# Kernel tuning notes

Hardware: AMD Instinct MI355X
Metric: run time of the kernel (lower is better)

## Reference

```python
import jax, jax.numpy as jnp
import numpy as np
from jax.scipy.special import logsumexp

V, C, S, H = 32000, 4096, 32, 512
B, T = 32, 256
NEG = jnp.float32(-1e10)  # masked_fill value used by mask_emission


def _res(x, w1, b1, w2, b2):
    # ResidualLayerOld: relu(lin1(x)); relu(lin2(h) + x)
    h = jax.nn.relu(x @ w1.T + b1)
    return jax.nn.relu(h @ w2.T + b2 + x)


def setup_inputs() -> dict:
    key = jax.random.key(0)
    ks = jax.random.split(key, 16)
    g = lambda i, shape, s=0.02: jax.random.normal(ks[i], shape, jnp.float32) * s
    return {
        "text": jax.random.randint(ks[0], (B, T), 0, V),
        "word2state": jax.random.randint(ks[1], (V, S), 0, C - 1),
        "start_emb": g(2, (C, H), 1.0),
        "start_w1": g(3, (H, H)), "start_b1": jnp.zeros((H,), jnp.float32),
        "start_w2": g(4, (H, H)), "start_b2": jnp.zeros((H,), jnp.float32),
        "start_w3": g(5, (1, H)), "start_b3": jnp.zeros((1,), jnp.float32),
        "state_emb": g(6, (C, H), 1.0),
        "trans_w1": g(7, (H, H)), "trans_b1": jnp.zeros((H,), jnp.float32),
        "trans_w2": g(8, (H, H)), "trans_b2": jnp.zeros((H,), jnp.float32),
        "next_state_proj": g(9, (C, H)),
        "preterminal_emb": g(10, (C, H), 1.0),
        "term_w1": g(11, (H, H)), "term_b1": jnp.zeros((H,), jnp.float32),
        "term_w2": g(12, (H, H)), "term_b2": jnp.zeros((H,), jnp.float32),
        "term_w3": g(13, (V, H)), "term_b3": jnp.zeros((V,), jnp.float32),
    }


def _forward(text, word2state, start_emb, start_w1, start_b1, start_w2, start_b2,
             start_w3, start_b3, state_emb, trans_w1, trans_b1, trans_w2, trans_b2,
             next_state_proj, preterminal_emb, term_w1, term_b1, term_w2, term_b2,
             term_w3, term_b3):
    ninf = -jnp.inf
    # start distribution over states [C]
    start = jax.nn.log_softmax(
        (_res(start_emb, start_w1, start_b1, start_w2, start_b2) @ start_w3.T + start_b3)[:, 0])
    # transition [C, C]: mask last column, row-normalize, mask last row (pad state)
    tl = _res(state_emb, trans_w1, trans_b1, trans_w2, trans_b2) @ next_state_proj.T
    tl = tl.at[:, -1].set(ninf)
    trans = jax.nn.log_softmax(tl, axis=-1)
    trans = jnp.where(jnp.isnan(trans), ninf, trans)
    trans = trans.at[-1, :].set(ninf)
    # emission [C, V]: sparse word2state mask, normalize over vocab
    el = _res(preterminal_emb, term_w1, term_b1, term_w2, term_b2) @ term_w3.T + term_b3
    emask = jnp.zeros((C, V), bool).at[
        word2state.reshape(-1), jnp.repeat(jnp.arange(V), S)].set(True)
    emit = jax.nn.log_softmax(jnp.where(emask, el, NEG), axis=-1)
    emit = jnp.where(jnp.isnan(emit), ninf, emit)
    emit = emit.at[-1, :].set(ninf)
    # clamp to the S states allowed for each observed word
    cs = word2state[text]                                  # [B, T, S]
    pot = trans[cs[:, :-1, :, None], cs[:, 1:, None, :]]   # [B, T-1, S, S] (cur, next)
    obs = emit[cs, text[:, :, None]]                       # [B, T, S]
    init = start[cs[:, 0]]                                 # [B, S]
    pot = pot + obs[:, 1:, None, :]                        # obs at t+1 on next axis
    pot = pot.at[:, 0].add(init[:, :, None] + obs[:, 0, :, None])
    pot = jnp.swapaxes(pot, -1, -2)                        # [B, T-1, next, prev]
    # log-domain forward scan (the fb kernel's alpha recursion)
    alpha0 = logsumexp(pot[:, 0], axis=-1)                 # [B, S]
    def step(alpha, p):
        return logsumexp(p + alpha[:, None, :], axis=-1), None
    alpha, _ = jax.lax.scan(step, alpha0, jnp.swapaxes(pot[:, 1:], 0, 1))
    return logsumexp(alpha, axis=-1).sum()                 # evidence (sum over batch)


def reference(text, word2state, start_emb, start_w1, start_b1, start_w2, start_b2,
              start_w3, start_b3, state_emb, trans_w1, trans_b1, trans_w2, trans_b2,
              next_state_proj, preterminal_emb, term_w1, term_b1, term_w2, term_b2,
              term_w3, term_b3):
    return _forward(text, word2state, start_emb, start_w1, start_b1, start_w2,
                    start_b2, start_w3, start_b3, state_emb, trans_w1, trans_b1,
                    trans_w2, trans_b2, next_state_proj, preterminal_emb, term_w1,
                    term_b1, term_w2, term_b2, term_w3, term_b3)
```

## Files before the change

kernel.cpp:

```cpp
#include <hip/hip_runtime.h>
#include <hip/hip_bf16.h>
#include <math.h>

#define NV 32000
#define NC 4096
#define NS 32
#define NH 512
#define NB 32
#define NT 256

typedef short s16x8 __attribute__((ext_vector_type(8)));
typedef float f32x4 __attribute__((ext_vector_type(4)));

__device__ __forceinline__ float wredMax(float v){
  #pragma unroll
  for (int o = 32; o; o >>= 1) v = fmaxf(v, __shfl_xor(v, o, 64));
  return v;
}
__device__ __forceinline__ float wredSum(float v){
  #pragma unroll
  for (int o = 32; o; o >>= 1) v += __shfl_xor(v, o, 64);
  return v;
}
__device__ __forceinline__ int f2ord(float f){ int i = __float_as_int(f); return i >= 0 ? i : (i ^ 0x7fffffff); }
__device__ __forceinline__ float ord2f(int i){ return __int_as_float(i >= 0 ? i : (i ^ 0x7fffffff)); }

__device__ __forceinline__ unsigned short f2bf(float x){
  unsigned int u = __float_as_uint(x);
  return (unsigned short)((u + 0x7fffu + ((u >> 16) & 1u)) >> 16);
}
__device__ __forceinline__ float bf2f(unsigned short h){
  return __uint_as_float((unsigned int)h << 16);
}

__device__ __forceinline__ void conv_body(const float* __restrict__ src,
                                          unsigned short* __restrict__ dst, int idx)
{
  const float* s = src + (size_t)idx * 8;
  float4 f0 = *(const float4*)s;
  float4 f1 = *(const float4*)(s + 4);
  float fv[8] = {f0.x, f0.y, f0.z, f0.w, f1.x, f1.y, f1.z, f1.w};
  s16x8 vh, vl;
  #pragma unroll
  for (int e = 0; e < 8; ++e) {
    unsigned short h = f2bf(fv[e]);
    vh[e] = (short)h;
    vl[e] = (short)f2bf(fv[e] - bf2f(h));
  }
  int r = idx >> 6, c8 = idx & 63;
  unsigned short* d = dst + (size_t)r * 1024 + c8 * 8;
  *(s16x8*)d = vh;
  *(s16x8*)(d + 512) = vl;
}

struct ConvArgs {
  const float* src[10];
  unsigned short* dst[10];
  int rows[10];
};

__global__ __launch_bounds__(256)
void conv_batch(ConvArgs a)
{
  int z = blockIdx.y;
  int idx = blockIdx.x * 256 + threadIdx.x;
  if (idx >= a.rows[z] * 64) return;
  conv_body(a.src[z], a.dst[z], idx);
}

__global__ __launch_bounds__(256)
void conv_single(const float* __restrict__ src, unsigned short* __restrict__ dst)
{
  int idx = blockIdx.x * 256 + threadIdx.x;
  conv_body(src, dst, idx);
}

template<int BM, bool RELU, bool BIAS, bool RES>
__global__ __launch_bounds__(256)
void gemm_bf16s(const unsigned short* __restrict__ Asp, const unsigned short* __restrict__ Bsp,
                const float* __restrict__ bias, const float* __restrict__ res,
                float* __restrict__ Co, int M, int N, int K)
{
  constexpr int BN = 128;
  constexpr int MF = BM / 32;
  constexpr int NFR = 4;
  __shared__ char smem[BM * 128 + BN * 128];
  char* smA = smem;
  char* smB = smem + BM * 128;

  const int tid  = threadIdx.x;
  const int lane = tid & 63, w = tid >> 6;
  const int wr = w >> 1, wc = w & 1;
  const int bm = blockIdx.y * BM, bn = blockIdx.x * BN;
  const int lda = 2 * K;
  const int l8 = lane >> 3, s8 = lane & 7;
  const int frow = lane & 15, kgrp = lane >> 4;

  f32x4 acc[MF][NFR] = {};

  #pragma unroll 1
  for (int seg = 0; seg < 3; ++seg) {
    const int aoff = (seg == 1) ? K : 0;
    const int boff = (seg == 2) ? K : 0;
    #pragma unroll 1
    for (int k0 = 0; k0 < K; k0 += 64) {
      #pragma unroll
      for (int c = 0; c < MF; ++c) {
        int q = w * MF + c;
        int row = q * 8 + l8;
        s16x8 v = *(const s16x8*)(Asp + (size_t)(bm + row) * lda + aoff + k0 + s8 * 8);
        unsigned int o = (unsigned int)(row * 128 + (s8 << 4));
        o ^= (unsigned int)((row & 7) << 4);
        *(s16x8*)(smA + o) = v;
      }
      #pragma unroll
      for (int c = 0; c < NFR; ++c) {
        int q = w * NFR + c;
        int row = q * 8 + l8;
        s16x8 v = *(const s16x8*)(Bsp + (size_t)(bn + row) * lda + boff + k0 + s8 * 8);
        unsigned int o = (unsigned int)(row * 128 + (s8 << 4));
        o ^= (unsigned int)((row & 7) << 4);
        *(s16x8*)(smB + o) = v;
      }
      __syncthreads();
      #pragma unroll
      for (int kk = 0; kk < 64; kk += 32) {
        s16x8 af[MF], bfr[NFR];
        #pragma unroll
        for (int im = 0; im < MF; ++im) {
          int ar = wr * (BM / 2) + im * 16 + frow;
          unsigned int o = ((unsigned int)(ar * 128 + (kk + kgrp * 8) * 2)) ^ ((unsigned int)((ar & 7) << 4));
          af[im] = *(const s16x8*)(smA + o);
        }
        #pragma unroll
        for (int jn = 0; jn < NFR; ++jn) {
          int bc = wc * 64 + jn * 16 + frow;
          unsigned int o = ((unsigned int)(bc * 128 + (kk + kgrp * 8) * 2)) ^ ((unsigned int)((bc & 7) << 4));
          bfr[jn] = *(const s16x8*)(smB + o);
        }
        #pragma unroll
        for (int im = 0; im < MF; ++im)
          #pragma unroll
          for (int jn = 0; jn < NFR; ++jn)
            asm volatile("v_mfma_f32_16x16x32_bf16 %0, %1, %2, %0"
                         : "+v"(acc[im][jn]) : "v"(af[im]), "v"(bfr[jn]));
      }
      __syncthreads();
    }
  }
  asm volatile("s_nop 7\n\ts_nop 7" ::: );
  #pragma unroll
  for (int im = 0; im < MF; ++im) {
    int row0 = bm + wr * (BM / 2) + im * 16 + kgrp * 4;
    #pragma unroll
    for (int jn = 0; jn < NFR; ++jn) {
      int col = bn + wc * 64 + jn * 16 + frow;
      #pragma unroll
      for (int j = 0; j < 4; ++j) {
        int r = row0 + j;
        float v = acc[im][jn][j];
        if constexpr (BIAS) v += bias[col];
        if constexpr (RES)  v += res[(size_t)r * N + col];
        if constexpr (RELU) v = fmaxf(v, 0.f);
        Co[(size_t)r * N + col] = v;
      }
    }
  }
}

__global__ __launch_bounds__(64)
void dot_head(const float* __restrict__ hS, const float* __restrict__ w3,
              const float* __restrict__ b3, float* __restrict__ sv)
{
  int c = blockIdx.x, lane = threadIdx.x;
  const float* hrow = hS + (size_t)c * NH;
  float acc = 0.f;
  #pragma unroll
  for (int e = 0; e < 8; ++e) acc += hrow[lane + e*64] * w3[lane + e*64];
  acc = wredSum(acc);
  if (lane == 0) sv[c] = acc + b3[0];
}

__global__ __launch_bounds__(1024)
void lse_vec(const float* __restrict__ x, int n, float* __restrict__ out)
{
  int tid = threadIdx.x;
  __shared__ float sm[16], ss[16];
  float m = -INFINITY;
  for (int i = tid; i < n; i += 1024) m = fmaxf(m, x[i]);
  m = wredMax(m);
  if ((tid & 63) == 0) sm[tid >> 6] = m;
  __syncthreads();
  m = sm[0];
  #pragma unroll
  for (int wv = 1; wv < 16; ++wv) m = fmaxf(m, sm[wv]);
  float s = 0.f;
  for (int i = tid; i < n; i += 1024) s += expf(x[i] - m);
  s = wredSum(s);
  if ((tid & 63) == 0) ss[tid >> 6] = s;
  __syncthreads();
  if (tid == 0) {
    float tot = 0.f;
    #pragma unroll
    for (int wv = 0; wv < 16; ++wv) tot += ss[wv];
    out[0] = m + logf(tot);
  }
}

__global__ __launch_bounds__(256)
void row_lse_trans(const float* __restrict__ tl, float* __restrict__ lse_t)
{
  int c = blockIdx.x;
  const float* row = tl + (size_t)c * NC;
  int tid = threadIdx.x;
  __shared__ float sm[4], ss[4];
  float m = -INFINITY;
  for (int n = tid; n < NC - 1; n += 256) m = fmaxf(m, row[n]);
  m = wredMax(m);
  if ((tid & 63) == 0) sm[tid >> 6] = m;
  __syncthreads();
  m = fmaxf(fmaxf(sm[0], sm[1]), fmaxf(sm[2], sm[3]));
  float s = 0.f;
  for (int n = tid; n < NC - 1; n += 256) s += expf(row[n] - m);
  s = wredSum(s);
  if ((tid & 63) == 0) ss[tid >> 6] = s;
  __syncthreads();
  if (tid == 0) lse_t[c] = m + logf(ss[0] + ss[1] + ss[2] + ss[3]);
}

__global__ __launch_bounds__(256)
void el_kernel(const int* __restrict__ w2s, const float* __restrict__ hP,
               const float* __restrict__ w3, const float* __restrict__ b3,
               float* __restrict__ el_g, unsigned int* __restrict__ vmask)
{
  int v = blockIdx.x;
  __shared__ float w3v[NH];
  __shared__ int crow[NS];
  int tid = threadIdx.x;
  if (tid < NS) crow[tid] = w2s[(size_t)v * NS + tid];
  for (int e = tid; e < NH; e += 256) w3v[e] = w3[(size_t)v * NH + e];
  __syncthreads();
  if (tid < 64) {
    bool valid = false;
    if (tid < NS) {
      valid = true;
      int c = crow[tid];
      for (int s2 = 0; s2 < tid; ++s2) if (crow[s2] == c) { valid = false; break; }
    }
    unsigned long long bal = __ballot(valid);
    if (tid == 0) vmask[v] = (unsigned int)(bal & 0xffffffffull);
  }
  int wave = tid >> 6, lane = tid & 63;
  float b3v = b3[v];
  #pragma unroll
  for (int q = 0; q < 8; ++q) {
    int s = wave * 8 + q;
    int c = crow[s];
    const float* hrow = hP + (size_t)c * NH;
    float acc = 0.f;
    #pragma unroll
    for (int e = 0; e < 8; ++e) acc += hrow[lane + e*64] * w3v[lane + e*64];
    acc = wredSum(acc);
    if (lane == 0) el_g[(size_t)v * NS + s] = acc + b3v;
  }
}

__global__ __launch_bounds__(256)
void init_e(int* __restrict__ emax, unsigned long long* __restrict__ esum)
{
  int i = blockIdx.x * 256 + threadIdx.x;
  if (i < NC) { emax[i] = 0x80000000; esum[i] = 0ull; }
}
__global__ __launch_bounds__(256)
void emit_max_k(const int* __restrict__ w2s, const float* __restrict__ el_g,
                const unsigned int* __restrict__ vmask, int* __restrict__ emax)
{
  int idx = blockIdx.x * 256 + threadIdx.x;
  int v = idx >> 5, s = idx & 31;
  if (!((vmask[v] >> s) & 1u)) return;
  atomicMax(&emax[w2s[idx]], f2ord(el_g[idx]));
}
__global__ __launch_bounds__(256)
void emit_sum_k(const int* __restrict__ w2s, const float* __restrict__ el_g,
                const unsigned int* __restrict__ vmask, const int* __restrict__ emax,
                unsigned long long* __restrict__ esum)
{
  int idx = blockIdx.x * 256 + threadIdx.x;
  int v = idx >> 5, s = idx & 31;
  if (!((vmask[v] >> s) & 1u)) return;
  int c = w2s[idx];
  float p = expf(el_g[idx] - ord2f(emax[c]));
  atomicAdd(&esum[c], (unsigned long long)(p * 0x1p40f));
}
__global__ __launch_bounds__(256)
void emit_fin_k(const int* __restrict__ emax, const unsigned long long* __restrict__ esum,
                float* __restrict__ lse_e)
{
  int c = blockIdx.x * 256 + threadIdx.x;
  if (c < NC) lse_e[c] = ord2f(emax[c]) + logf((float)esum[c] * 0x1p-40f);
}

__global__ __launch_bounds__(256)
void build_cs(const int* __restrict__ text, const int* __restrict__ w2s,
              unsigned short* __restrict__ cs_all)
{
  int idx = blockIdx.x * 256 + threadIdx.x;
  int s = idx & 31;
  int bt = idx >> 5;
  int v = text[bt];
  cs_all[idx] = (unsigned short)w2s[(size_t)v * NS + s];
}

__global__ __launch_bounds__(1024)
void gather_pot(const unsigned short* __restrict__ cs_all, const float* __restrict__ tl,
                float* __restrict__ pot)
{
  int t = blockIdx.x;
  int b = blockIdx.y;
  int tid = threadIdx.x;
  __shared__ unsigned short c1s[NS], c2s[NS];
  if (tid < NS) c1s[tid] = cs_all[((size_t)b * NT + t) * NS + tid];
  else if (tid < 2 * NS) c2s[tid - NS] = cs_all[((size_t)b * NT + t + 1) * NS + (tid - NS)];
  __syncthreads();
  int gi = tid >> 5, gj = tid & 31;
  float v = tl[(size_t)c1s[gi] * NC + c2s[gj]];
  pot[((size_t)b * (NT - 1) + t) * 1024 + gj * 32 + gi] = v;
}

__global__ __launch_bounds__(1024)
void scan_kernel(const int* __restrict__ text, const int* __restrict__ w2s,
                 const float* __restrict__ pot, const float* __restrict__ lse_t,
                 const float* __restrict__ sv, const float* __restrict__ lse_st,
                 const float* __restrict__ el_g, const float* __restrict__ lse_e,
                 float* __restrict__ out_b)
{
  int b = blockIdx.x;
  __shared__ unsigned short cs[NT][NS];
  __shared__ float D[NT][NS];
  __shared__ float beta[NS];
  __shared__ float alpha_out[NS];
  __shared__ int textb[NT];
  int tid = threadIdx.x;

  if (tid < NT) textb[tid] = text[b * NT + tid];
  __syncthreads();
  for (int idx = tid; idx < NT * NS; idx += 1024) {
    int t = idx >> 5, s = idx & 31;
    int v = textb[t];
    int c = w2s[v * NS + s];
    cs[t][s] = (unsigned short)c;
    D[t][s] = el_g[(size_t)v * NS + s] - lse_e[c] - lse_t[c];
  }
  __syncthreads();
  if (tid < NS) {
    int c0 = cs[0][tid];
    beta[tid] = sv[c0] - lse_st[0] + D[0][tid];
  }
  __syncthreads();

  const int j = tid >> 5, i = tid & 31;
  const float* potb = pot + (size_t)b * (NT - 1) * 1024;
  float val_next = potb[tid];
  for (int t = 0; t < NT - 1; ++t) {
    float val = val_next;
    if (t < NT - 2) val_next = potb[(size_t)(t + 1) * 1024 + tid];
    float x = val + beta[i];
    float m = x;
    #pragma unroll
    for (int o = 16; o; o >>= 1) m = fmaxf(m, __shfl_xor(m, o, 32));
    float p = expf(x - m);
    #pragma unroll
    for (int o = 16; o; o >>= 1) p += __shfl_xor(p, o, 32);
    float r = m + logf(p);
    __syncthreads();
    if (i == 0) {
      if (t < NT - 2) beta[j] = r + D[t+1][j];
      else alpha_out[j] = r + D[t+1][j] + lse_t[cs[t+1][j]];
    }
    __syncthreads();
  }

  if (tid < 32) {
    float a = alpha_out[tid];
    float m = a;
    #pragma unroll
    for (int o = 16; o; o >>= 1) m = fmaxf(m, __shfl_xor(m, o, 32));
    float p = expf(a - m);
    #pragma unroll
    for (int o = 16; o; o >>= 1) p += __shfl_xor(p, o, 32);
    if (tid == 0) out_b[b] = m + logf(p);
  }
}

__global__ void final_sum(const float* __restrict__ out_b, float* __restrict__ out)
{
  if (threadIdx.x == 0) {
    float s = 0.f;
    for (int b = 0; b < NB; ++b) s += out_b[b];
    out[0] = s;
  }
}

extern "C" void kernel_launch(void* const* d_in, const int* in_sizes, int n_in,
                              void* d_out, int out_size, void* d_ws, size_t ws_size,
                              hipStream_t stream)
{
  (void)in_sizes; (void)n_in; (void)out_size; (void)ws_size;
  const int*   text      = (const int*)d_in[0];
  const int*   w2s       = (const int*)d_in[1];
  const float* start_emb = (const float*)d_in[2];
  const float* start_w1  = (const float*)d_in[3];
  const float* start_b1  = (const float*)d_in[4];
  const float* start_w2  = (const float*)d_in[5];
  const float* start_b2  = (const float*)d_in[6];
  const float* start_w3  = (const float*)d_in[7];
  const float* start_b3  = (const float*)d_in[8];
  const float* state_emb = (const float*)d_in[9];
  const float* trans_w1  = (const float*)d_in[10];
  const float* trans_b1  = (const float*)d_in[11];
  const float* trans_w2  = (const float*)d_in[12];
  const float* trans_b2  = (const float*)d_in[13];
  const float* nsp       = (const float*)d_in[14];
  const float* pre_emb   = (const float*)d_in[15];
  const float* term_w1   = (const float*)d_in[16];
  const float* term_b1   = (const float*)d_in[17];
  const float* term_w2   = (const float*)d_in[18];
  const float* term_b2   = (const float*)d_in[19];
  const float* term_w3   = (const float*)d_in[20];
  const float* term_b3   = (const float*)d_in[21];

  float* tl    = (float*)d_ws;
  float* h1    = tl + 16777216;
  float* h2    = h1 + 2097152;
  float* sv    = h2 + 2097152;
  float* lse_t = sv + NC;
  float* lse_e = lse_t + NC;
  float* lse_s = lse_e + NC;
  float* out_b = lse_s + 64;
  float* el_g  = out_b + 64;
  unsigned int* vmask = (unsigned int*)(el_g + 1024000);
  int* emax    = (int*)(vmask + 32000);
  unsigned long long* esum = (unsigned long long*)(emax + 4096);
  unsigned short* sE_s  = (unsigned short*)(esum + 4096);
  unsigned short* tE_s  = sE_s  + 4194304;
  unsigned short* pE_s  = tE_s  + 4194304;
  unsigned short* nsp_s = pE_s  + 4194304;
  unsigned short* h1_s  = nsp_s + 4194304;
  unsigned short* w1S_s = h1_s  + 4194304;
  unsigned short* w2S_s = w1S_s + 524288;
  unsigned short* w1T_s = w2S_s + 524288;
  unsigned short* w2T_s = w1T_s + 524288;
  unsigned short* w1P_s = w2T_s + 524288;
  unsigned short* w2P_s = w1P_s + 524288;
  unsigned short* cs_all = w2P_s + 524288;
  unsigned short* h2t_s = sE_s;
  float* pot = (float*)sE_s;

  ConvArgs ca;
  ca.src[0]=start_emb; ca.dst[0]=sE_s;  ca.rows[0]=NC;
  ca.src[1]=state_emb; ca.dst[1]=tE_s;  ca.rows[1]=NC;
  ca.src[2]=pre_emb;   ca.dst[2]=pE_s;  ca.rows[2]=NC;
  ca.src[3]=nsp;       ca.dst[3]=nsp_s; ca.rows[3]=NC;
  ca.src[4]=start_w1;  ca.dst[4]=w1S_s; ca.rows[4]=NH;
  ca.src[5]=start_w2;  ca.dst[5]=w2S_s; ca.rows[5]=NH;
  ca.src[6]=trans_w1;  ca.dst[6]=w1T_s; ca.rows[6]=NH;
  ca.src[7]=trans_w2;  ca.dst[7]=w2T_s; ca.rows[7]=NH;
  ca.src[8]=term_w1;   ca.dst[8]=w1P_s; ca.rows[8]=NH;
  ca.src[9]=term_w2;   ca.dst[9]=w2P_s; ca.rows[9]=NH;
  conv_batch<<<dim3(1024, 10), 256, 0, stream>>>(ca);

  dim3 blk(256);
  dim3 gHH(4, 64);
  dim3 gCC(32, 32);

  gemm_bf16s<64, true,  true,  false><<<gHH, blk, 0, stream>>>(sE_s, w1S_s, start_b1, nullptr,   h1, NC, NH, NH);
  conv_single<<<1024, 256, 0, stream>>>(h1, h1_s);
  gemm_bf16s<64, true,  true,  true ><<<gHH, blk, 0, stream>>>(h1_s, w2S_s, start_b2, start_emb, h2, NC, NH, NH);
  dot_head<<<NC, 64, 0, stream>>>(h2, start_w3, start_b3, sv);
  lse_vec<<<1, 1024, 0, stream>>>(sv, NC, lse_s);

  gemm_bf16s<64, true,  true,  false><<<gHH, blk, 0, stream>>>(tE_s, w1T_s, trans_b1, nullptr,   h1, NC, NH, NH);
  conv_single<<<1024, 256, 0, stream>>>(h1, h1_s);
  gemm_bf16s<64, true,  true,  true ><<<gHH, blk, 0, stream>>>(h1_s, w2T_s, trans_b2, state_emb, h2, NC, NH, NH);
  conv_single<<<1024, 256, 0, stream>>>(h2, h2t_s);
  gemm_bf16s<128, false, false, false><<<gCC, blk, 0, stream>>>(h2t_s, nsp_s, nullptr, nullptr, tl, NC, NC, NH);
  row_lse_trans<<<NC, 256, 0, stream>>>(tl, lse_t);

  gemm_bf16s<64, true,  true,  false><<<gHH, blk, 0, stream>>>(pE_s, w1P_s, term_b1, nullptr,  h1, NC, NH, NH);
  conv_single<<<1024, 256, 0, stream>>>(h1, h1_s);
  gemm_bf16s<64, true,  true,  true ><<<gHH, blk, 0, stream>>>(h1_s, w2P_s, term_b2, pre_emb,  h2, NC, NH, NH);
  el_kernel<<<NV, 256, 0, stream>>>(w2s, h2, term_w3, term_b3, el_g, vmask);
  init_e<<<16, 256, 0, stream>>>(emax, esum);
  emit_max_k<<<NV * NS / 256, 256, 0, stream>>>(w2s, el_g, vmask, emax);
  emit_sum_k<<<NV * NS / 256, 256, 0, stream>>>(w2s, el_g, vmask, emax, esum);
  emit_fin_k<<<NC / 256, 256, 0, stream>>>(emax, esum, lse_e);

  build_cs<<<NB * NT * NS / 256, 256, 0, stream>>>(text, w2s, cs_all);
  gather_pot<<<dim3(NT - 1, NB), 1024, 0, stream>>>(cs_all, tl, pot);

  scan_kernel<<<NB, 1024, 0, stream>>>(text, w2s, pot, lse_t, sv, lse_s, el_g, lse_e, out_b);
  final_sum<<<1, 64, 0, stream>>>(out_b, (float*)d_out);
}
```

Before: 959.5 us.

## Batch residual GEMMs, fuse bf16 split into epilogue, rewrite scan as single-wave

The three H×H residual-layer GEMM pairs now run as two batched launches over a z dimension. Their epilogues write the hi/lo bf16 split directly, which removes the separate conv_single passes and the fp32 intermediates. The per-timestep emission terms D, the initial beta and the final offset are precomputed in a parallel build_D kernel. The forward scan becomes a 64-thread single-wave kernel that uses shuffles instead of shared memory and __syncthreads, and double-buffers the pot loads. The trade-off is a reshuffled workspace layout with aliasing and fast-math __expf/__logf in the recurrence.

```diff
diff --git a/kernel.cpp b/kernel.cpp
--- a/kernel.cpp
+++ b/kernel.cpp
@@ -68,17 +68,9 @@
   conv_body(a.src[z], a.dst[z], idx);
 }
 
-__global__ __launch_bounds__(256)
-void conv_single(const float* __restrict__ src, unsigned short* __restrict__ dst)
-{
-  int idx = blockIdx.x * 256 + threadIdx.x;
-  conv_body(src, dst, idx);
-}
-
-template<int BM, bool RELU, bool BIAS, bool RES>
+template<int BM>
 __global__ __launch_bounds__(256)
 void gemm_bf16s(const unsigned short* __restrict__ Asp, const unsigned short* __restrict__ Bsp,
-                const float* __restrict__ bias, const float* __restrict__ res,
                 float* __restrict__ Co, int M, int N, int K)
 {
   constexpr int BN = 128;
@@ -156,13 +148,117 @@
     for (int jn = 0; jn < NFR; ++jn) {
       int col = bn + wc * 64 + jn * 16 + frow;
       #pragma unroll
+      for (int j = 0; j < 4; ++j)
+        Co[(size_t)(row0 + j) * N + col] = acc[im][jn][j];
+    }
+  }
+}
+
+struct G3 {
+  const unsigned short* A[3];
+  const unsigned short* B[3];
+  const float* bias[3];
+  const float* res[3];
+  float* Cf[3];
+  unsigned short* Cs[3];
+};
+
+template<bool RES>
+__global__ __launch_bounds__(256)
+void gemm3(G3 a)
+{
+  constexpr int BM = 64, BN = 128, K = 512, N = 512;
+  constexpr int MF = 2, NFR = 4;
+  __shared__ char smem[BM * 128 + BN * 128];
+  char* smA = smem;
+  char* smB = smem + BM * 128;
+
+  const int z = blockIdx.z;
+  const unsigned short* Asp = a.A[z];
+  const unsigned short* Bsp = a.B[z];
+  const float* bias = a.bias[z];
+  float* Cf = a.Cf[z];
+  unsigned short* Cs = a.Cs[z];
+
+  const int tid  = threadIdx.x;
+  const int lane = tid & 63, w = tid >> 6;
+  const int wr = w >> 1, wc = w & 1;
+  const int bm = blockIdx.y * BM, bn = blockIdx.x * BN;
+  const int lda = 2 * K;
+  const int l8 = lane >> 3, s8 = lane & 7;
+  const int frow = lane & 15, kgrp = lane >> 4;
+
+  f32x4 acc[MF][NFR] = {};
+
+  #pragma unroll 1
+  for (int seg = 0; seg < 3; ++seg) {
+    const int aoff = (seg == 1) ? K : 0;
+    const int boff = (seg == 2) ? K : 0;
+    #pragma unroll 1
+    for (int k0 = 0; k0 < K; k0 += 64) {
+      #pragma unroll
+      for (int c = 0; c < MF; ++c) {
+        int q = w * MF + c;
+        int row = q * 8 + l8;
+        s16x8 v = *(const s16x8*)(Asp + (size_t)(bm + row) * lda + aoff + k0 + s8 * 8);
+        unsigned int o = (unsigned int)(row * 128 + (s8 << 4));
+        o ^= (unsigned int)((row & 7) << 4);
+        *(s16x8*)(smA + o) = v;
+      }
+      #pragma unroll
+      for (int c = 0; c < NFR; ++c) {
+        int q = w * NFR + c;
+        int row = q * 8 + l8;
+        s16x8 v = *(const s16x8*)(Bsp + (size_t)(bn + row) * lda + boff + k0 + s8 * 8);
+        unsigned int o = (unsigned int)(row * 128 + (s8 << 4));
+        o ^= (unsigned int)((row & 7) << 4);
+        *(s16x8*)(smB + o) = v;
+      }
+      __syncthreads();
+      #pragma unroll
+      for (int kk = 0; kk < 64; kk += 32) {
+        s16x8 af[MF], bfr[NFR];
+        #pragma unroll
+        for (int im = 0; im < MF; ++im) {
+          int ar = wr * (BM / 2) + im * 16 + frow;
+          unsigned int o = ((unsigned int)(ar * 128 + (kk + kgrp * 8) * 2)) ^ ((unsigned int)((ar & 7) << 4));
+          af[im] = *(const s16x8*)(smA + o);
+        }
+        #pragma unroll
+        for (int jn = 0; jn < NFR; ++jn) {
+          int bc = wc * 64 + jn * 16 + frow;
+          unsigned int o = ((unsigned int)(bc * 128 + (kk + kgrp * 8) * 2)) ^ ((unsigned int)((bc & 7) << 4));
+          bfr[jn] = *(const s16x8*)(smB + o);
+        }
+        #pragma unroll
+        for (int im = 0; im < MF; ++im)
+          #pragma unroll
+          for (int jn = 0; jn < NFR; ++jn)
+            asm volatile("v_mfma_f32_16x16x32_bf16 %0, %1, %2, %0"
+                         : "+v"(acc[im][jn]) : "v"(af[im]), "v"(bfr[jn]));
+      }
+      __syncthreads();
+    }
+  }
+  asm volatile("s_nop 7\n\ts_nop 7" ::: );
+  #pragma unroll
+  for (int im = 0; im < MF; ++im) {
+    int row0 = bm + wr * (BM / 2) + im * 16 + kgrp * 4;
+    #pragma unroll
+    for (int jn = 0; jn < NFR; ++jn) {
+      int col = bn + wc * 64 + jn * 16 + frow;
+      #pragma unroll
       for (int j = 0; j < 4; ++j) {
         int r = row0 + j;
-        float v = acc[im][jn][j];
-        if constexpr (BIAS) v += bias[col];
-        if constexpr (RES)  v += res[(size_t)r * N + col];
-        if constexpr (RELU) v = fmaxf(v, 0.f);
-        Co[(size_t)r * N + col] = v;
+        float v = acc[im][jn][j] + bias[col];
+        if constexpr (RES) v += a.res[z][(size_t)r * N + col];
+        v = fmaxf(v, 0.f);
+        if (Cf) Cf[(size_t)r * N + col] = v;
+        if (Cs) {
+          unsigned short hi = f2bf(v);
+          Cs[(size_t)r * 1024 + col] = hi;
+          Cs[(size_t)r * 1024 + 512 + col] = f2bf(v - bf2f(hi));
+        }
       }
     }
   }
@@ -301,14 +397,25 @@
 }
 
 __global__ __launch_bounds__(256)
-void build_cs(const int* __restrict__ text, const int* __restrict__ w2s,
-              unsigned short* __restrict__ cs_all)
+void build_D(const int* __restrict__ text, const int* __restrict__ w2s,
+             const float* __restrict__ el_g, const float* __restrict__ lse_e,
+             const float* __restrict__ lse_t, const float* __restrict__ sv,
+             const float* __restrict__ lse_s,
+             float* __restrict__ Dall, float* __restrict__ Dlast,
+             float* __restrict__ beta0, unsigned short* __restrict__ cs_all)
 {
   int idx = blockIdx.x * 256 + threadIdx.x;
   int s = idx & 31;
   int bt = idx >> 5;
+  int t = bt & (NT - 1);
+  int b = bt >> 8;
   int v = text[bt];
-  cs_all[idx] = (unsigned short)w2s[(size_t)v * NS + s];
+  int c = w2s[(size_t)v * NS + s];
+  cs_all[idx] = (unsigned short)c;
+  float D = el_g[(size_t)v * NS + s] - lse_e[c] - lse_t[c];
+  Dall[idx] = D;
+  if (t == NT - 1) Dlast[b * NS + s] = D + lse_t[c];
+  if (t == 0)      beta0[b * NS + s] = sv[c] - lse_s[0] + D;
 }
 
 __global__ __launch_bounds__(1024)
@@ -327,69 +434,90 @@
   pot[((size_t)b * (NT - 1) + t) * 1024 + gj * 32 + gi] = v;
 }
 
-__global__ __launch_bounds__(1024)
-void scan_kernel(const int* __restrict__ text, const int* __restrict__ w2s,
-                 const float* __restrict__ pot, const float* __restrict__ lse_t,
-                 const float* __restrict__ sv, const float* __restrict__ lse_st,
-                 const float* __restrict__ el_g, const float* __restrict__ lse_e,
+__device__ __forceinline__ float lse_step(float4 p0, float4 p1, float4 p2, float4 p3,
+                                          float beta, int h16)
+{
+  float pv[16] = {p0.x,p0.y,p0.z,p0.w, p1.x,p1.y,p1.z,p1.w,
+                  p2.x,p2.y,p2.z,p2.w, p3.x,p3.y,p3.z,p3.w};
+  float xs[16];
+  #pragma unroll
+  for (int q = 0; q < 16; ++q)
+    xs[q] = pv[q] + __shfl(beta, h16 + q, 64);
+  float a[8];
+  #pragma unroll
+  for (int q = 0; q < 8; ++q) a[q] = fmaxf(xs[q], xs[q + 8]);
+  float c4[4];
+  #pragma unroll
+  for (int q = 0; q < 4; ++q) c4[q] = fmaxf(a[q], a[q + 4]);
+  float m = fmaxf(fmaxf(c4[0], c4[1]), fmaxf(c4[2], c4[3]));
+  m = fmaxf(m, __shfl_xor(m, 32, 64));
+  float e[8];
+  #pragma unroll
+  for (int q = 0; q < 8; ++q) e[q] = __expf(xs[q] - m) + __expf(xs[q + 8] - m);
+  float s4[4];
+  #pragma unroll
+  for (int q = 0; q < 4; ++q) s4[q] = e[q] + e[q + 4];
+  float st = (s4[0] + s4[1]) + (s4[2] + s4[3]);
+  st += __shfl_xor(st, 32, 64);
+  return m + __logf(st);
+}
+
+__global__ __launch_bounds__(64)
+void scan_kernel(const float* __restrict__ pot, const float* __restrict__ Dall,
+                 const float* __restrict__ Dlast, const float* __restrict__ beta0,
                  float* __restrict__ out_b)
 {
-  int b = blockIdx.x;
-  __shared__ unsigned short cs[NT][NS];
-  __shared__ float D[NT][NS];
-  __shared__ float beta[NS];
-  __shared__ float alpha_out[NS];
-  __shared__ int textb[NT];
-  int tid = threadIdx.x;
-
-  if (tid < NT) textb[tid] = text[b * NT + tid];
-  __syncthreads();
-  for (int idx = tid; idx < NT * NS; idx += 1024) {
-    int t = idx >> 5, s = idx & 31;
-    int v = textb[t];
-    int c = w2s[v * NS + s];
-    cs[t][s] = (unsigned short)c;
-    D[t][s] = el_g[(size_t)v * NS + s] - lse_e[c] - lse_t[c];
-  }
-  __syncthreads();
-  if (tid < NS) {
-    int c0 = cs[0][tid];
-    beta[tid] = sv[c0] - lse_st[0] + D[0][tid];
-  }
-  __syncthreads();
-
-  const int j = tid >> 5, i = tid & 31;
-  const float* potb = pot + (size_t)b * (NT - 1) * 1024;
-  float val_next = potb[tid];
-  for (int t = 0; t < NT - 1; ++t) {
-    float val = val_next;
-    if (t < NT - 2) val_next = potb[(size_t)(t + 1) * 1024 + tid];
-    float x = val + beta[i];
-    float m = x;
-    #pragma unroll
-    for (int o = 16; o; o >>= 1) m = fmaxf(m, __shfl_xor(m, o, 32));
-    float p = expf(x - m);
-    #pragma unroll
-    for (int o = 16; o; o >>= 1) p += __shfl_xor(p, o, 32);
-    float r = m + logf(p);
-    __syncthreads();
-    if (i == 0) {
-      if (t < NT - 2) beta[j] = r + D[t+1][j];
-      else alpha_out[j] = r + D[t+1][j] + lse_t[cs[t+1][j]];
-    }
-    __syncthreads();
-  }
-
-  if (tid < 32) {
-    float a = alpha_out[tid];
-    float m = a;
-    #pragma unroll
-    for (int o = 16; o; o >>= 1) m = fmaxf(m, __shfl_xor(m, o, 32));
-    float p = expf(a - m);
-    #pragma unroll
-    for (int o = 16; o; o >>= 1) p += __shfl_xor(p, o, 32);
-    if (tid == 0) out_b[b] = m + logf(p);
-  }
+  const int b = blockIdx.x;
+  const int lane = threadIdx.x;
+  const int j = lane & 31;
+  const int h16 = (lane >> 5) * 16;
+  const float* potb = pot + (size_t)b * (NT - 1) * 1024 + j * 32 + h16;
+  const float* Db = Dall + (size_t)b * NT * NS + j;
+
+  float beta = beta0[b * NS + j];
+
+  float4 A0 = *(const float4*)(potb + 0);
+  float4 A1 = *(const float4*)(potb + 4);
+  float4 A2 = *(const float4*)(potb + 8);
+  float4 A3 = *(const float4*)(potb + 12);
+  const float* pB0 = potb + 1024;
+  float4 B0 = *(const float4*)(pB0 + 0);
+  float4 B1 = *(const float4*)(pB0 + 4);
+  float4 B2 = *(const float4*)(pB0 + 8);
+  float4 B3 = *(const float4*)(pB0 + 12);
+  float dA = Db[1 * NS];
+  float dB = Db[2 * NS];
+
+  #pragma unroll 1
+  for (int t = 0; t < NT - 2; t += 2) {
+    float r = lse_step(A0, A1, A2, A3, beta, h16);
+    beta = r + dA;
+    const float* pn = potb + (size_t)(t + 2) * 1024;
+    A0 = *(const float4*)(pn + 0);
+    A1 = *(const float4*)(pn + 4);
+    A2 = *(const float4*)(pn + 8);
+    A3 = *(const float4*)(pn + 12);
+    dA = Db[(t + 3 < NT ? t + 3 : NT - 1) * NS];
+    float r2 = lse_step(B0, B1, B2, B3, beta, h16);
+    beta = r2 + dB;
+    int tb = (t + 3 < NT - 1) ? t + 3 : NT - 2;
+    const float* pn2 = potb + (size_t)tb * 1024;
+    B0 = *(const float4*)(pn2 + 0);
+    B1 = *(const float4*)(pn2 + 4);
+    B2 = *(const float4*)(pn2 + 8);
+    B3 = *(const float4*)(pn2 + 12);
+    dB = Db[(t + 4 < NT ? t + 4 : NT - 1) * NS];
+  }
+  float r = lse_step(A0, A1, A2, A3, beta, h16);
+  float rfin = r + Dlast[b * NS + j];
+
+  float m = rfin;
+  #pragma unroll
+  for (int o = 16; o; o >>= 1) m = fmaxf(m, __shfl_xor(m, o, 32));
+  float p = expf(rfin - m);
+  #pragma unroll
+  for (int o = 16; o; o >>= 1) p += __shfl_xor(p, o, 32);
+  if (lane == 0) out_b[b] = m + logf(p);
 }
 
 __global__ void final_sum(const float* __restrict__ out_b, float* __restrict__ out)
@@ -430,31 +558,36 @@
   const float* term_b3   = (const float*)d_in[21];
 
   float* tl    = (float*)d_ws;
-  float* h1    = tl + 16777216;
-  float* h2    = h1 + 2097152;
-  float* sv    = h2 + 2097152;
-  float* lse_t = sv + NC;
-  float* lse_e = lse_t + NC;
-  float* lse_s = lse_e + NC;
+  float* el_g  = tl + 16777216;
+  float* sv    = el_g + 1024000;
+  float* lse_t = sv + 4096;
+  float* lse_e = lse_t + 4096;
+  float* lse_s = lse_e + 4096;
   float* out_b = lse_s + 64;
-  float* el_g  = out_b + 64;
-  unsigned int* vmask = (unsigned int*)(el_g + 1024000);
-  int* emax    = (int*)(vmask + 32000);
+  float* Dlast = out_b + 64;
+  float* beta0 = Dlast + 1024;
+  unsigned int* vmask = (unsigned int*)(beta0 + 1024);
+  int* emax = (int*)(vmask + 32768);
   unsigned long long* esum = (unsigned long long*)(emax + 4096);
   unsigned short* sE_s  = (unsigned short*)(esum + 4096);
   unsigned short* tE_s  = sE_s  + 4194304;
   unsigned short* pE_s  = tE_s  + 4194304;
   unsigned short* nsp_s = pE_s  + 4194304;
-  unsigned short* h1_s  = nsp_s + 4194304;
-  unsigned short* w1S_s = h1_s  + 4194304;
+  unsigned short* w1S_s = nsp_s + 4194304;
   unsigned short* w2S_s = w1S_s + 524288;
   unsigned short* w1T_s = w2S_s + 524288;
   unsigned short* w2T_s = w1T_s + 524288;
   unsigned short* w1P_s = w2T_s + 524288;
   unsigned short* w2P_s = w1P_s + 524288;
-  unsigned short* cs_all = w2P_s + 524288;
-  unsigned short* h2t_s = sE_s;
-  float* pot = (float*)sE_s;
+  unsigned short* h1s0  = w2P_s + 524288;
+  unsigned short* h1s1  = h1s0 + 4194304;
+  unsigned short* h1s2  = h1s1 + 4194304;
+  float* h2f0 = (float*)sE_s;
+  unsigned short* h2s1 = tE_s;
+  float* h2f2 = (float*)pE_s;
+  float* pot  = (float*)sE_s;
+  float* Dall = (float*)h1s0;
+  unsigned short* cs_all = (unsigned short*)((char*)h1s0 + 1048576);
 
   ConvArgs ca;
   ca.src[0]=start_emb; ca.dst[0]=sE_s;  ca.rows[0]=NC;
@@ -469,35 +602,40 @@
   ca.src[9]=term_w2;   ca.dst[9]=w2P_s; ca.rows[9]=NH;
   conv_batch<<<dim3(1024, 10), 256, 0, stream>>>(ca);
 
-  dim3 blk(256);
-  dim3 gHH(4, 64);
-  dim3 gCC(32, 32);
-
-  gemm_bf16s<64, true,  true,  false><<<gHH, blk, 0, stream>>>(sE_s, w1S_s, start_b1, nullptr,   h1, NC, NH, NH);
-  conv_single<<<1024, 256, 0, stream>>>(h1, h1_s);
-  gemm_bf16s<64, true,  true,  true ><<<gHH, blk, 0, stream>>>(h1_s, w2S_s, start_b2, start_emb, h2, NC, NH, NH);
-  dot_head<<<NC, 64, 0, stream>>>(h2, start_w3, start_b3, sv);
+  G3 g1;
+  g1.A[0]=sE_s;  g1.A[1]=tE_s;  g1.A[2]=pE_s;
+  g1.B[0]=w1S_s; g1.B[1]=w1T_s; g1.B[2]=w1P_s;
+  g1.bias[0]=start_b1; g1.bias[1]=trans_b1; g1.bias[2]=term_b1;
+  g1.res[0]=nullptr; g1.res[1]=nullptr; g1.res[2]=nullptr;
+  g1.Cf[0]=nullptr; g1.Cf[1]=nullptr; g1.Cf[2]=nullptr;
+  g1.Cs[0]=h1s0; g1.Cs[1]=h1s1; g1.Cs[2]=h1s2;
+  gemm3<false><<<dim3(4, 64, 3), 256, 0, stream>>>(g1);
+
+  G3 g2;
+  g2.A[0]=h1s0;  g2.A[1]=h1s1;  g2.A[2]=h1s2;
+  g2.B[0]=w2S_s; g2.B[1]=w2T_s; g2.B[2]=w2P_s;
+  g2.bias[0]=start_b2; g2.bias[1]=trans_b2; g2.bias[2]=term_b2;
+  g2.res[0]=start_emb; g2.res[1]=state_emb; g2.res[2]=pre_emb;
+  g2.Cf[0]=h2f0; g2.Cf[1]=nullptr; g2.Cf[2]=h2f2;
+  g2.Cs[0]=nullptr; g2.Cs[1]=h2s1; g2.Cs[2]=nullptr;
+  gemm3<true><<<dim3(4, 64, 3), 256, 0, stream>>>(g2);
+
+  dot_head<<<NC, 64, 0, stream>>>(h2f0, start_w3, start_b3, sv);
   lse_vec<<<1, 1024, 0, stream>>>(sv, NC, lse_s);
 
-  gemm_bf16s<64, true,  true,  false><<<gHH, blk, 0, stream>>>(tE_s, w1T_s, trans_b1, nullptr,   h1, NC, NH, NH);
-  conv_single<<<1024, 256, 0, stream>>>(h1, h1_s);
-  gemm_bf16s<64, true,  true,  true ><<<gHH, blk, 0, stream>>>(h1_s, w2T_s, trans_b2, state_emb, h2, NC, NH, NH);
-  conv_single<<<1024, 256, 0, stream>>>(h2, h2t_s);
-  gemm_bf16s<128, false, false, false><<<gCC, blk, 0, stream>>>(h2t_s, nsp_s, nullptr, nullptr, tl, NC, NC, NH);
+  gemm_bf16s<128><<<dim3(32, 32), 256, 0, stream>>>(h2s1, nsp_s, tl, NC, NC, NH);
   row_lse_trans<<<NC, 256, 0, stream>>>(tl, lse_t);
 
-  gemm_bf16s<64, true,  true,  false><<<gHH, blk, 0, stream>>>(pE_s, w1P_s, term_b1, nullptr,  h1, NC, NH, NH);
-  conv_single<<<1024, 256, 0, stream>>>(h1, h1_s);
-  gemm_bf16s<64, true,  true,  true ><<<gHH, blk, 0, stream>>>(h1_s, w2P_s, term_b2, pre_emb,  h2, NC, NH, NH);
-  el_kernel<<<NV, 256, 0, stream>>>(w2s, h2, term_w3, term_b3, el_g, vmask);
+  el_kernel<<<NV, 256, 0, stream>>>(w2s, h2f2, term_w3, term_b3, el_g, vmask);
   init_e<<<16, 256, 0, stream>>>(emax, esum);
   emit_max_k<<<NV * NS / 256, 256, 0, stream>>>(w2s, el_g, vmask, emax);
   emit_sum_k<<<NV * NS / 256, 256, 0, stream>>>(w2s, el_g, vmask, emax, esum);
   emit_fin_k<<<NC / 256, 256, 0, stream>>>(emax, esum, lse_e);
 
-  build_cs<<<NB * NT * NS / 256, 256, 0, stream>>>(text, w2s, cs_all);
+  build_D<<<NB * NT * NS / 256, 256, 0, stream>>>(text, w2s, el_g, lse_e, lse_t, sv, lse_s,
+                                                  Dall, Dlast, beta0, cs_all);
   gather_pot<<<dim3(NT - 1, NB), 1024, 0, stream>>>(cs_all, tl, pot);
 
-  scan_kernel<<<NB, 1024, 0, stream>>>(text, w2s, pot, lse_t, sv, lse_s, el_g, lse_e, out_b);
+  scan_kernel<<<NB, 64, 0, stream>>>(pot, Dall, Dlast, beta0, out_b);
   final_sum<<<1, 64, 0, stream>>>(out_b, (float*)d_out);
 }
```

Result: faster. 899.1 us (-6.3%).
